# Kernel tuning notes

Measured on AMD Instinct MI355X. Metric: run time of the kernel, lower is better.

## Reference

```python
import jax, jax.numpy as jnp
import numpy as np

B, T, C, H = 2, 2048, 1024, 16
HD = C // H  # 64
EPS = 1e-5


def _ln(x, g, b):
    mu = jnp.mean(x, axis=-1, keepdims=True)
    var = jnp.var(x, axis=-1, keepdims=True)
    return (x - mu) * jax.lax.rsqrt(var + EPS) * g + b


def setup_inputs() -> dict:
    key = jax.random.key(0)
    ks = jax.random.split(key, 8)
    s = lambda n: 1.0 / np.sqrt(n)
    return {
        "x": jax.random.normal(ks[0], (B, T, C), dtype=jnp.float32),
        "ln1_g": jnp.ones((C,), jnp.float32), "ln1_b": jnp.zeros((C,), jnp.float32),
        "ln2_g": jnp.ones((C,), jnp.float32), "ln2_b": jnp.zeros((C,), jnp.float32),
        "w_in": jax.random.normal(ks[1], (C, 3 * C), jnp.float32) * s(C),
        "b_in": jnp.zeros((3 * C,), jnp.float32),
        "w_out": jax.random.normal(ks[2], (C, C), jnp.float32) * s(C),
        "b_out": jnp.zeros((C,), jnp.float32),
        "w_fc": jax.random.normal(ks[3], (C, 4 * C), jnp.float32) * s(C),
        "b_fc": jnp.zeros((4 * C,), jnp.float32),
        "w_proj": jax.random.normal(ks[4], (4 * C, C), jnp.float32) * s(4 * C),
        "b_proj": jnp.zeros((C,), jnp.float32),
    }


def reference(x, ln1_g, ln1_b, ln2_g, ln2_b, w_in, b_in, w_out, b_out,
              w_fc, b_fc, w_proj, b_proj):
    # --- residual 1: x + attn(ln1(x)) ---
    h = _ln(x, ln1_g, ln1_b)
    qkv = h @ w_in + b_in                          # (B,T,3C)
    # reshape to (B,T,H,3*HD) then chunk per head (matches torch code exactly)
    qkv = qkv.reshape(B, T, H, 3 * HD).transpose(0, 2, 1, 3)  # (B,H,T,3*HD)
    q, k, v = jnp.split(qkv, 3, axis=-1)           # each (B,H,T,HD)
    att = jnp.einsum('bhqd,bhkd->bhqk', q, k) / np.sqrt(HD)
    causal = jnp.tril(jnp.ones((T, T), bool))
    att = jnp.where(causal, att, -jnp.inf)
    att = jax.nn.softmax(att, axis=-1)
    o = jnp.einsum('bhqk,bhkd->bhqd', att, v)      # (B,H,T,HD)
    o = o.transpose(0, 2, 1, 3).reshape(B, T, C)
    x1 = x + (o @ w_out + b_out)
    # --- ln2 applied to residual stream, then residual 2 on top of ln2 output ---
    y = _ln(x1, ln2_g, ln2_b)
    mlp = jax.nn.gelu(y @ w_fc + b_fc, approximate=False) @ w_proj + b_proj
    return y + mlp
```

## Files before the change

kernel.cpp:

```cpp
#include <hip/hip_runtime.h>
#include <hip/hip_bf16.h>
#include <math.h>

typedef __bf16 bf16;
typedef __bf16 bf16x8 __attribute__((ext_vector_type(8)));
typedef __bf16 bf16x4 __attribute__((ext_vector_type(4)));
typedef float floatx4 __attribute__((ext_vector_type(4)));

#define B_ 2
#define T_ 2048
#define C_ 1024
#define H_ 16
#define HD_ 64


__device__ __forceinline__ void gload_lds16(const bf16* g, bf16* l) {
    __builtin_amdgcn_global_load_lds(
        (const __attribute__((address_space(1))) unsigned int*)(g),
        (__attribute__((address_space(3))) unsigned int*)(l), 16, 0, 0);
}

__global__ __launch_bounds__(256) void transpose_all(
        const float* __restrict__ w_in, const float* __restrict__ w_out,
        const float* __restrict__ w_fc, const float* __restrict__ w_proj,
        bf16* __restrict__ o_in, bf16* __restrict__ o_out,
        bf16* __restrict__ o_fc, bf16* __restrict__ o_proj) {
    __shared__ float shf[64 * 33];
    int t = blockIdx.x;
    int tid = threadIdx.x;
    if (t < 7168) {
        const float* src; bf16* dst; int K, N, idx;
        if (t < 3072) { src = w_in; dst = o_in; K = 1024; N = 3072; idx = t; }
        else          { src = w_fc; dst = o_fc; K = 1024; N = 4096; idx = t - 3072; }
        int ntx = N >> 5;
        int nt = (idx % ntx) * 32, kt = (idx / ntx) * 32;
        int tx = tid & 31, ty = tid >> 5;
        #pragma unroll
        for (int i = 0; i < 32; i += 8)
            shf[(ty + i) * 33 + tx] = src[(size_t)(kt + ty + i) * N + nt + tx];
        __syncthreads();
        #pragma unroll
        for (int i = 0; i < 32; i += 8)
            dst[(size_t)(nt + ty + i) * K + kt + tx] = (bf16)shf[tx * 33 + ty + i];
    } else {
        const float* src; bf16* dst; int K, idx;
        if (t < 7680) { src = w_out;  dst = o_out;  K = 1024; idx = t - 7168; }
        else          { src = w_proj; dst = o_proj; K = 4096; idx = t - 7680; }
        const int N = 1024;
        int n0 = (idx & 31) * 32, k0 = (idx >> 5) * 64;
        int col = tid & 31, kr = tid >> 5;
        #pragma unroll
        for (int s = 0; s < 8; s++)
            shf[(kr + s * 8) * 33 + col] = src[(size_t)(k0 + kr + s * 8) * N + n0 + col];
        __syncthreads();
        int tl = tid >> 6, l = tid & 63;
        int ntl = tl & 1, kcl = tl >> 1;
        int rr = ntl * 16 + (l & 15);
        int qd = l >> 4;
        bf16x8 v;
        #pragma unroll
        for (int e = 0; e < 8; e++)
            v[e] = (bf16)shf[(kcl * 32 + qd * 8 + e) * 33 + rr];
        size_t nt_g = (n0 >> 4) + ntl, kc_g = (k0 >> 5) + kcl;
        *(bf16x8*)(dst + (nt_g * (K >> 5) + kc_g) * 512 + l * 8) = v;
    }
}

__global__ __launch_bounds__(256) void ln_kernel(const float* __restrict__ x,
                                                 const float* __restrict__ g,
                                                 const float* __restrict__ b,
                                                 bf16* __restrict__ out_b,
                                                 float* __restrict__ out_f) {
    int row = blockIdx.x;
    int tid = threadIdx.x;
    const float* xr = x + (size_t)row * C_;
    float4 v = ((const float4*)xr)[tid];
    float s  = v.x + v.y + v.z + v.w;
    float ss = v.x * v.x + v.y * v.y + v.z * v.z + v.w * v.w;
    #pragma unroll
    for (int off = 32; off; off >>= 1) {
        s  += __shfl_down(s, off);
        ss += __shfl_down(ss, off);
    }
    __shared__ float red[8];
    int wid = tid >> 6;
    if ((tid & 63) == 0) { red[wid] = s; red[wid + 4] = ss; }
    __syncthreads();
    s  = red[0] + red[1] + red[2] + red[3];
    ss = red[4] + red[5] + red[6] + red[7];
    float mean = s * (1.0f / C_);
    float var  = ss * (1.0f / C_) - mean * mean;
    float rstd = rsqrtf(var + 1e-5f);
    float4 gv = ((const float4*)g)[tid];
    float4 bv = ((const float4*)b)[tid];
    float o0 = (v.x - mean) * rstd * gv.x + bv.x;
    float o1 = (v.y - mean) * rstd * gv.y + bv.y;
    float o2 = (v.z - mean) * rstd * gv.z + bv.z;
    float o3 = (v.w - mean) * rstd * gv.w + bv.w;
    bf16x4 ob = { (bf16)o0, (bf16)o1, (bf16)o2, (bf16)o3 };
    ((bf16x4*)out_b)[(size_t)row * 256 + tid] = ob;
    if (out_f) {
        float4 of; of.x = o0; of.y = o1; of.z = o2; of.w = o3;
        ((float4*)out_f)[(size_t)row * 256 + tid] = of;
    }
}

__device__ __forceinline__ float gelu_fast(float x) {
    float z2 = 1.5957691216f * (x + 0.044715f * x * x * x);
    float e = __expf(z2);
    float t = 1.0f - 2.0f * __builtin_amdgcn_rcpf(e + 1.0f);
    return 0.5f * x * (1.0f + t);
}

#define BAR() do { __builtin_amdgcn_sched_barrier(0); __builtin_amdgcn_s_barrier(); __builtin_amdgcn_sched_barrier(0); } while (0)
#define VMC6() asm volatile("s_waitcnt vmcnt(6)" ::: "memory")
#define VMC0() asm volatile("s_waitcnt vmcnt(0)" ::: "memory")

#define LOAD_A(AS, QM) \
  { _Pragma("unroll") for (int i_ = 0; i_ < 4; i_++) { \
      const int r_ = wm128 + ((QM) * 4 + i_) * 16 + lm; \
      _Pragma("unroll") for (int kc_ = 0; kc_ < 2; kc_++) \
        aR[i_][kc_] = *(const bf16x8*)((AS) + r_ * 64 + ((((kc_ << 2) | quad) ^ (lm & 7)) << 3)); } }

#define LOAD_B(BS, QN) \
  { _Pragma("unroll") for (int j_ = 0; j_ < 2; j_++) { \
      const int r_ = wn64 + ((QN) * 2 + j_) * 16 + lm; \
      _Pragma("unroll") for (int kc_ = 0; kc_ < 2; kc_++) \
        bR[QN][j_][kc_] = *(const bf16x8*)((BS) + r_ * 64 + ((((kc_ << 2) | quad) ^ (lm & 7)) << 3)); } }

#define MFMA_Q(QM, QN) \
  { __builtin_amdgcn_s_setprio(1); \
    _Pragma("unroll") for (int i_ = 0; i_ < 4; i_++) \
    _Pragma("unroll") for (int j_ = 0; j_ < 2; j_++) \
    _Pragma("unroll") for (int kc_ = 0; kc_ < 2; kc_++) \
      acc[(QM) * 4 + i_][(QN) * 2 + j_] = __builtin_amdgcn_mfma_f32_16x16x32_bf16( \
          aR[i_][kc_], bR[QN][j_][kc_], acc[(QM) * 4 + i_][(QN) * 2 + j_], 0, 0, 0); \
    __builtin_amdgcn_s_setprio(0); }

#define STG(gb, lb, r0v, k0v) \
    gload_lds16((gb) + (size_t)((r0v) + sr8) * K + (k0v) + scb, (lb) + ((r0v) + wid * 8) * 64)

template<int MODE>
__global__ __launch_bounds__(512, 2) void gemm256(const bf16* __restrict__ A,
                                                  const bf16* __restrict__ Bt,
                                                  const float* __restrict__ bias,
                                                  void* __restrict__ out,
                                                  int M, int N, int K) {
    (void)M;
    __shared__ __align__(16) bf16 smem[4 * 256 * 64];
    bf16* As0 = smem;
    bf16* Bs0 = smem + 1 * 256 * 64;
    bf16* As1 = smem + 2 * 256 * 64;
    bf16* Bs1 = smem + 3 * 256 * 64;

    int ntn = N >> 8;
    int lin = blockIdx.x;
    int id  = (lin & 7) * (gridDim.x >> 3) + (lin >> 3);
    int mt = id / ntn, nt = id - mt * ntn;
    int m0 = mt << 8, n0 = nt << 8;

    int tid = threadIdx.x;
    int wid = __builtin_amdgcn_readfirstlane(tid >> 6);
    int lane = tid & 63;
    int lm = lane & 15, quad = lane >> 4;
    int wm128 = (wid & 1) * 128;
    int wn64  = (wid >> 1) * 64;

    const bf16* Ablk = A  + (size_t)m0 * K;
    const bf16* Bblk = Bt + (size_t)n0 * K;

    int sr8 = wid * 8 + (lane >> 3);
    int scb = ((lane & 7) ^ (lane >> 3)) << 3;

    floatx4 acc[8][4];
    #pragma unroll
    for (int f = 0; f < 8; f++)
        #pragma unroll
        for (int g = 0; g < 4; g++) { floatx4 z = {0.f, 0.f, 0.f, 0.f}; acc[f][g] = z; }
    bf16x8 aR[4][2], bR[2][2][2];

    int nI = K >> 7;

    STG(Ablk, As0, 0, 0);   STG(Ablk, As0, 64, 0);
    STG(Ablk, As0, 128, 0); STG(Ablk, As0, 192, 0);
    STG(Bblk, Bs0, 0, 0);   STG(Bblk, Bs0, 64, 0);
    STG(Bblk, Bs0, 128, 0); STG(Bblk, Bs0, 192, 0);
    STG(Ablk, As1, 0, 64);  STG(Ablk, As1, 128, 64);
    STG(Bblk, Bs1, 0, 64);  STG(Bblk, Bs1, 64, 64);
    STG(Ablk, As1, 64, 64); STG(Ablk, As1, 192, 64);
    VMC6();
    BAR();

    for (int it = 0; it < nI; it++) {
        int kE = (2 * it + 2) << 6;
        int kO = (2 * it + 3) << 6;
        int kT = (2 * it + 1) << 6;
        bool nl = (it + 1 < nI);
        LOAD_A(As0, 0); LOAD_B(Bs0, 0);
        STG(Bblk, Bs1, 128, kT); STG(Bblk, Bs1, 192, kT);
        BAR(); MFMA_Q(0, 0); BAR();
        LOAD_B(Bs0, 1);
        if (nl) { STG(Ablk, As0, 0, kE); STG(Ablk, As0, 128, kE); }
        BAR(); MFMA_Q(0, 1); BAR();
        LOAD_A(As0, 1);
        if (nl) { STG(Bblk, Bs0, 0, kE); STG(Bblk, Bs0, 64, kE); }
        BAR(); MFMA_Q(1, 0); BAR();
        if (nl) { STG(Ablk, As0, 64, kE); STG(Ablk, As0, 192, kE); }
        BAR(); MFMA_Q(1, 1);
        if (nl) { VMC6(); } else { VMC0(); }
        BAR();
        LOAD_A(As1, 0); LOAD_B(Bs1, 0);
        if (nl) { STG(Bblk, Bs0, 128, kE); STG(Bblk, Bs0, 192, kE); }
        BAR(); MFMA_Q(0, 0); BAR();
        LOAD_B(Bs1, 1);
        if (nl) { STG(Ablk, As1, 0, kO); STG(Ablk, As1, 128, kO); }
        BAR(); MFMA_Q(0, 1); BAR();
        LOAD_A(As1, 1);
        if (nl) { STG(Bblk, Bs1, 0, kO); STG(Bblk, Bs1, 64, kO); }
        BAR(); MFMA_Q(1, 0); BAR();
        if (nl) { STG(Ablk, As1, 64, kO); STG(Ablk, As1, 192, kO); }
        BAR(); MFMA_Q(1, 1);
        if (nl) { VMC6(); }
        BAR();
    }

    if (MODE == 0) {
        bf16* ob = (bf16*)out;
        #pragma unroll
        for (int f = 0; f < 8; f++) {
            int row0 = m0 + wm128 + f * 16 + quad * 4;
            #pragma unroll
            for (int g = 0; g < 4; g++) {
                int n = n0 + wn64 + g * 16 + lm;
                float bsn = bias[n];
                #pragma unroll
                for (int r = 0; r < 4; r++)
                    ob[(size_t)(row0 + r) * N + n] = (bf16)(acc[f][g][r] + bsn);
            }
        }
    } else {
        bf16* ob = (bf16*)out;
        bf16* patch = smem + wid * (64 * 68);
        size_t mtb = (size_t)((m0 + wm128) >> 4);
        int ncb = (n0 + wn64) >> 5;
        #pragma unroll
        for (int h = 0; h < 2; h++) {
            #pragma unroll
            for (int ff = 0; ff < 4; ff++)
                #pragma unroll
                for (int g = 0; g < 4; g++) {
                    int n = n0 + wn64 + g * 16 + lm;
                    float bsn = bias[n];
                    #pragma unroll
                    for (int r = 0; r < 4; r++)
                        patch[(ff * 16 + quad * 4 + r) * 68 + g * 16 + lm] =
                            (bf16)gelu_fast(acc[h * 4 + ff][g][r] + bsn);
                }
            #pragma unroll
            for (int ff = 0; ff < 4; ff++)
                #pragma unroll
                for (int kc = 0; kc < 2; kc++) {
                    bf16x8 v = *(const bf16x8*)&patch[(ff * 16 + lm) * 68 + kc * 32 + quad * 8];
                    size_t tile = (mtb + h * 4 + ff) * (size_t)(N >> 5) + ncb + kc;
                    *(bf16x8*)(ob + tile * 512 + lane * 8) = v;
                }
        }
    }
}

#define GD_STEP(BUF, SS) \
  if ((SS) < S) { \
    int kp_ = 2 * (SS) + 4; \
    if (kp_ < KC) { \
      _Pragma("unroll") for (int i_ = 0; i_ < 4; i_++) \
        _Pragma("unroll") for (int c_ = 0; c_ < 2; c_++) \
          ab[((BUF) + 2) % 3][i_][c_] = *(const bf16x8*)(Ab + ((size_t)i_ * KC + kp_ + c_) * 512); \
      _Pragma("unroll") for (int j_ = 0; j_ < 2; j_++) \
        _Pragma("unroll") for (int c_ = 0; c_ < 2; c_++) \
          bb[((BUF) + 2) % 3][j_][c_] = *(const bf16x8*)(Bb + ((size_t)j_ * KC + kp_ + c_) * 512); \
    } \
    _Pragma("unroll") for (int c_ = 0; c_ < 2; c_++) \
      _Pragma("unroll") for (int i_ = 0; i_ < 4; i_++) \
        _Pragma("unroll") for (int j_ = 0; j_ < 2; j_++) \
          acc[i_][j_] = __builtin_amdgcn_mfma_f32_16x16x32_bf16(ab[BUF][i_][c_], bb[BUF][j_][c_], acc[i_][j_], 0, 0, 0); \
  }

__global__ __launch_bounds__(256, 2) void gemm_direct(const bf16* __restrict__ Af,
                                                      const bf16* __restrict__ Bf,
                                                      const float* __restrict__ bias,
                                                      const float* __restrict__ add,
                                                      float* __restrict__ out,
                                                      int M, int N, int K) {
    (void)M;
    int lin = blockIdx.x;
    int xcd = lin & 7, loc = lin >> 3;
    int m0 = ((xcd << 2) | (loc & 3)) * 128;
    int n0 = (loc >> 2) * 64;
    int tid = threadIdx.x;
    int wid = __builtin_amdgcn_readfirstlane(tid >> 6);
    int lane = tid & 63;
    int lm = lane & 15, quad = lane >> 4;
    int wm = (wid & 1) * 64, wn = (wid >> 1) * 32;
    int KC = K >> 5;
    const bf16* Ab = Af + ((size_t)((m0 + wm) >> 4) * KC) * 512 + lane * 8;
    const bf16* Bb = Bf + ((size_t)((n0 + wn) >> 4) * KC) * 512 + lane * 8;

    floatx4 acc[4][2];
    #pragma unroll
    for (int i = 0; i < 4; i++)
        #pragma unroll
        for (int j = 0; j < 2; j++) { floatx4 z = {0.f, 0.f, 0.f, 0.f}; acc[i][j] = z; }

    bf16x8 ab[3][4][2], bb[3][2][2];
    #pragma unroll
    for (int c = 0; c < 2; c++) {
        #pragma unroll
        for (int i = 0; i < 4; i++) {
            ab[0][i][c] = *(const bf16x8*)(Ab + ((size_t)i * KC + c) * 512);
            ab[1][i][c] = *(const bf16x8*)(Ab + ((size_t)i * KC + 2 + c) * 512);
        }
        #pragma unroll
        for (int j = 0; j < 2; j++) {
            bb[0][j][c] = *(const bf16x8*)(Bb + ((size_t)j * KC + c) * 512);
            bb[1][j][c] = *(const bf16x8*)(Bb + ((size_t)j * KC + 2 + c) * 512);
        }
    }

    int S = KC >> 1;
    for (int s0 = 0; s0 < S; s0 += 3) {
        GD_STEP(0, s0);
        GD_STEP(1, s0 + 1);
        GD_STEP(2, s0 + 2);
    }

    #pragma unroll
    for (int i = 0; i < 4; i++)
        #pragma unroll
        for (int j = 0; j < 2; j++) {
            int mbase = m0 + wm + i * 16 + quad * 4;
            int n     = n0 + wn + j * 16 + lm;
            float bsn = bias[n];
            #pragma unroll
            for (int r = 0; r < 4; r++) {
                size_t idx = (size_t)(mbase + r) * N + n;
                out[idx] = acc[i][j][r] + bsn + add[idx];
            }
        }
}

#define QT_ 128
#define KT_ 64

__global__ __launch_bounds__(512) void attn_mfma_kernel(const bf16* __restrict__ qkv,
                                                        bf16* __restrict__ of) {
    int bh = blockIdx.x;
    int b = bh >> 4, h = bh & 15;
    int q0 = (gridDim.y - 1 - blockIdx.y) * QT_;
    int tid = threadIdx.x, wid = tid >> 6, lane = tid & 63;
    int lm = lane & 15, quad = lane >> 4;
    int sw = lm & 7;
    int r0 = q0 + wid * 16;

    const bf16* base = qkv + (size_t)b * T_ * (3 * C_) + h * (3 * HD_);

    __shared__ __align__(16) bf16 Ks[KT_][72];
    __shared__ __align__(16) bf16 Vt[HD_][72];
    __shared__ __align__(16) bf16 PsT[8][16][64];

    bf16x8 qf[2];
    #pragma unroll
    for (int kc = 0; kc < 2; kc++) {
        bf16x8 t = *(const bf16x8*)(base + (size_t)(r0 + lm) * (3 * C_) + kc * 32 + quad * 8);
        #pragma unroll
        for (int e = 0; e < 8; e++) t[e] = (bf16)((float)t[e] * 0.125f);
        qf[kc] = t;
    }

    floatx4 acc_o[4];
    #pragma unroll
    for (int dn = 0; dn < 4; dn++) { floatx4 z = {0.f, 0.f, 0.f, 0.f}; acc_o[dn] = z; }
    float mst = -1e30f, lst = 0.0f;

    int srow = tid >> 3;
    int scol = (tid & 7) * 8;

    int kmax = q0 + QT_;
    for (int k0 = 0; k0 < kmax; k0 += KT_) {
        bf16x8 kv = *(const bf16x8*)(base + (size_t)(k0 + srow) * (3 * C_) + HD_ + scol);
        bf16x8 vv = *(const bf16x8*)(base + (size_t)(k0 + srow) * (3 * C_) + 2 * HD_ + scol);
        __syncthreads();
        *(bf16x8*)(&Ks[srow][scol]) = kv;
        {
            int c = scol >> 3;
            int pk = ((srow >> 3) ^ c) * 8 + (srow & 7);
            #pragma unroll
            for (int j = 0; j < 8; j++) Vt[scol + j][pk] = vv[j];
        }
        __syncthreads();

        if (k0 <= r0 + 15) {
            floatx4 st[4];
            #pragma unroll
            for (int bn = 0; bn < 4; bn++) { floatx4 z = {0.f, 0.f, 0.f, 0.f}; st[bn] = z; }
            #pragma unroll
            for (int kc = 0; kc < 2; kc++) {
                bf16x8 kf[4];
                #pragma unroll
                for (int bn = 0; bn < 4; bn++)
                    kf[bn] = *(const bf16x8*)(&Ks[bn * 16 + lm][kc * 32 + quad * 8]);
                #pragma unroll
                for (int bn = 0; bn < 4; bn++)
                    st[bn] = __builtin_amdgcn_mfma_f32_16x16x32_bf16(kf[bn], qf[kc], st[bn], 0, 0, 0);
            }

            float vv_[4][4];
            float rm = -1e30f;
            if (k0 + KT_ - 1 > r0) {
                int gq = r0 + lm;
                #pragma unroll
                for (int bn = 0; bn < 4; bn++)
                    #pragma unroll
                    for (int r = 0; r < 4; r++) {
                        int key = k0 + bn * 16 + quad * 4 + r;
                        float sv = (key <= gq) ? st[bn][r] : -1e30f;
                        vv_[bn][r] = sv;
                        rm = fmaxf(rm, sv);
                    }
            } else {
                #pragma unroll
                for (int bn = 0; bn < 4; bn++)
                    #pragma unroll
                    for (int r = 0; r < 4; r++) {
                        vv_[bn][r] = st[bn][r];
                        rm = fmaxf(rm, st[bn][r]);
                    }
            }
            rm = fmaxf(rm, __shfl_xor(rm, 16));
            rm = fmaxf(rm, __shfl_xor(rm, 32));
            float mnew = fmaxf(mst, rm);
            float alpha = __expf(mst - mnew);
            mst = mnew;
            float ps = 0.f;
            #pragma unroll
            for (int bn = 0; bn < 4; bn++) {
                float p0 = __expf(vv_[bn][0] - mnew);
                float p1 = __expf(vv_[bn][1] - mnew);
                float p2 = __expf(vv_[bn][2] - mnew);
                float p3 = __expf(vv_[bn][3] - mnew);
                ps += (p0 + p1) + (p2 + p3);
                bf16x4 pk = { (bf16)p0, (bf16)p1, (bf16)p2, (bf16)p3 };
                int kb = bn * 2 + (quad >> 1);
                int col = ((kb ^ sw) << 3) + (quad & 1) * 4;
                *(bf16x4*)(&PsT[wid][lm][col]) = pk;
            }
            ps += __shfl_xor(ps, 16);
            ps += __shfl_xor(ps, 32);
            lst = lst * alpha + ps;

            #pragma unroll
            for (int r = 0; r < 4; r++) {
                float ar = __shfl(alpha, quad * 4 + r);
                #pragma unroll
                for (int dn = 0; dn < 4; dn++) acc_o[dn][r] *= ar;
            }

            __asm__ volatile("s_waitcnt lgkmcnt(0)" ::: "memory");

            #pragma unroll
            for (int kc = 0; kc < 2; kc++) {
                bf16x8 pa = *(const bf16x8*)(&PsT[wid][lm][((kc * 4 + quad) ^ sw) << 3]);
                bf16x8 vfr[4];
                #pragma unroll
                for (int dn = 0; dn < 4; dn++) {
                    int d = dn * 16 + lm;
                    int swd = (d >> 3) & 7;
                    vfr[dn] = *(const bf16x8*)(&Vt[d][(((kc * 4 + quad) ^ swd) << 3)]);
                }
                #pragma unroll
                for (int dn = 0; dn < 4; dn++)
                    acc_o[dn] = __builtin_amdgcn_mfma_f32_16x16x32_bf16(pa, vfr[dn], acc_o[dn], 0, 0, 0);
            }
        }
    }

    float il = 1.0f / lst;
    #pragma unroll
    for (int r = 0; r < 4; r++) {
        float ir = __shfl(il, quad * 4 + r);
        #pragma unroll
        for (int dn = 0; dn < 4; dn++)
            PsT[wid][quad * 4 + r][dn * 16 + lm] = (bf16)(acc_o[dn][r] * ir);
    }
    __asm__ volatile("s_waitcnt lgkmcnt(0)" ::: "memory");
    size_t mtb = ((size_t)b * T_ + r0) >> 4;
    #pragma unroll
    for (int kcl = 0; kcl < 2; kcl++) {
        bf16x8 v = *(const bf16x8*)&PsT[wid][lm][kcl * 32 + quad * 8];
        *(bf16x8*)(of + (mtb * (C_ >> 5) + (h * 2 + kcl)) * 512 + lane * 8) = v;
    }
}

extern "C" void kernel_launch(void* const* d_in, const int* in_sizes, int n_in,
                              void* d_out, int out_size, void* d_ws, size_t ws_size,
                              hipStream_t stream) {
    (void)in_sizes; (void)n_in; (void)out_size; (void)ws_size;
    const float* x      = (const float*)d_in[0];
    const float* ln1_g  = (const float*)d_in[1];
    const float* ln1_b  = (const float*)d_in[2];
    const float* ln2_g  = (const float*)d_in[3];
    const float* ln2_b  = (const float*)d_in[4];
    const float* w_in   = (const float*)d_in[5];
    const float* b_in   = (const float*)d_in[6];
    const float* w_out  = (const float*)d_in[7];
    const float* b_out  = (const float*)d_in[8];
    const float* w_fc   = (const float*)d_in[9];
    const float* b_fc   = (const float*)d_in[10];
    const float* w_proj = (const float*)d_in[11];
    const float* b_proj = (const float*)d_in[12];

    char* ws = (char*)d_ws;
    const size_t MB = 1024 * 1024;
    bf16*  w_inT   = (bf16*)(ws + 0);
    bf16*  w_outF  = (bf16*)(ws + 6 * MB);
    bf16*  w_fcT   = (bf16*)(ws + 8 * MB);
    bf16*  w_projF = (bf16*)(ws + 16 * MB);
    bf16*  qkv     = (bf16*)(ws + 24 * MB);
    bf16*  fc_frag = (bf16*)(ws + 24 * MB);
    bf16*  o_frag  = (bf16*)(ws + 56 * MB);
    bf16*  y_b     = (bf16*)(ws + 56 * MB);
    bf16*  h_b     = (bf16*)(ws + 64 * MB);
    float* x1      = (float*)(ws + 64 * MB);
    float* y_f     = (float*)(ws + 80 * MB);

    const int M = B_ * T_;

    transpose_all<<<9728, 256, 0, stream>>>(w_in, w_out, w_fc, w_proj,
                                            w_inT, w_outF, w_fcT, w_projF);

    ln_kernel<<<M, 256, 0, stream>>>(x, ln1_g, ln1_b, h_b, nullptr);
    gemm256<0><<<(M >> 8) * ((3 * C_) >> 8), 512, 0, stream>>>(h_b, w_inT, b_in,
                                                               qkv, M, 3 * C_, C_);
    attn_mfma_kernel<<<dim3(B_ * H_, T_ / QT_), 512, 0, stream>>>(qkv, o_frag);
    gemm_direct<<<512, 256, 0, stream>>>(o_frag, w_outF, b_out, x, x1, M, C_, C_);
    ln_kernel<<<M, 256, 0, stream>>>(x1, ln2_g, ln2_b, y_b, y_f);
    gemm256<1><<<(M >> 8) * ((4 * C_) >> 8), 512, 0, stream>>>(y_b, w_fcT, b_fc,
                                                               fc_frag, M, 4 * C_, C_);
    gemm_direct<<<512, 256, 0, stream>>>(fc_frag, w_projF, b_proj, y_f,
                                         (float*)d_out, M, C_, 4 * C_);
}
```

Baseline: 330.0 us.

## Replace fragment-layout direct GEMM with LDS-pipelined row-major GEMM for out/proj

Drops the pre-swizzled MFMA fragment layout for the attention output, FC activations and the w_out/w_proj weights, and stores them all row-major. The two N=1024 GEMMs now use a new kernel that streams A and B through a 4-stage LDS ring filled by global_load_lds, uses XOR-swizzled reads and 128x128 tiles with 512 threads. It also raises wave priority around the MFMA blocks in both the GEMM and the attention kernel. The intent is to hide global-load latency behind compute and cut the register-resident pipeline pressure of the old direct kernel, at the cost of LDS traffic and a barrier every K step.

```diff
diff --git a/kernel.cpp b/kernel.cpp
--- a/kernel.cpp
+++ b/kernel.cpp
@@ -13,7 +13,6 @@
 #define H_ 16
 #define HD_ 64
 
-
 __device__ __forceinline__ void gload_lds16(const bf16* g, bf16* l) {
     __builtin_amdgcn_global_load_lds(
         (const __attribute__((address_space(1))) unsigned int*)(g),
@@ -25,45 +24,24 @@
         const float* __restrict__ w_fc, const float* __restrict__ w_proj,
         bf16* __restrict__ o_in, bf16* __restrict__ o_out,
         bf16* __restrict__ o_fc, bf16* __restrict__ o_proj) {
-    __shared__ float shf[64 * 33];
+    __shared__ float shf[32 * 33];
     int t = blockIdx.x;
     int tid = threadIdx.x;
-    if (t < 7168) {
-        const float* src; bf16* dst; int K, N, idx;
-        if (t < 3072) { src = w_in; dst = o_in; K = 1024; N = 3072; idx = t; }
-        else          { src = w_fc; dst = o_fc; K = 1024; N = 4096; idx = t - 3072; }
-        int ntx = N >> 5;
-        int nt = (idx % ntx) * 32, kt = (idx / ntx) * 32;
-        int tx = tid & 31, ty = tid >> 5;
-        #pragma unroll
-        for (int i = 0; i < 32; i += 8)
-            shf[(ty + i) * 33 + tx] = src[(size_t)(kt + ty + i) * N + nt + tx];
-        __syncthreads();
-        #pragma unroll
-        for (int i = 0; i < 32; i += 8)
-            dst[(size_t)(nt + ty + i) * K + kt + tx] = (bf16)shf[tx * 33 + ty + i];
-    } else {
-        const float* src; bf16* dst; int K, idx;
-        if (t < 7680) { src = w_out;  dst = o_out;  K = 1024; idx = t - 7168; }
-        else          { src = w_proj; dst = o_proj; K = 4096; idx = t - 7680; }
-        const int N = 1024;
-        int n0 = (idx & 31) * 32, k0 = (idx >> 5) * 64;
-        int col = tid & 31, kr = tid >> 5;
-        #pragma unroll
-        for (int s = 0; s < 8; s++)
-            shf[(kr + s * 8) * 33 + col] = src[(size_t)(k0 + kr + s * 8) * N + n0 + col];
-        __syncthreads();
-        int tl = tid >> 6, l = tid & 63;
-        int ntl = tl & 1, kcl = tl >> 1;
-        int rr = ntl * 16 + (l & 15);
-        int qd = l >> 4;
-        bf16x8 v;
-        #pragma unroll
-        for (int e = 0; e < 8; e++)
-            v[e] = (bf16)shf[(kcl * 32 + qd * 8 + e) * 33 + rr];
-        size_t nt_g = (n0 >> 4) + ntl, kc_g = (k0 >> 5) + kcl;
-        *(bf16x8*)(dst + (nt_g * (K >> 5) + kc_g) * 512 + l * 8) = v;
-    }
+    const float* src; bf16* dst; int K, N, idx;
+    if (t < 3072)      { src = w_in;   dst = o_in;   K = 1024; N = 3072; idx = t; }
+    else if (t < 7168) { src = w_fc;   dst = o_fc;   K = 1024; N = 4096; idx = t - 3072; }
+    else if (t < 8192) { src = w_out;  dst = o_out;  K = 1024; N = 1024; idx = t - 7168; }
+    else               { src = w_proj; dst = o_proj; K = 4096; N = 1024; idx = t - 8192; }
+    int ntx = N >> 5;
+    int nt = (idx % ntx) * 32, kt = (idx / ntx) * 32;
+    int tx = tid & 31, ty = tid >> 5;
+    #pragma unroll
+    for (int i = 0; i < 32; i += 8)
+        shf[(ty + i) * 33 + tx] = src[(size_t)(kt + ty + i) * N + nt + tx];
+    __syncthreads();
+    #pragma unroll
+    for (int i = 0; i < 32; i += 8)
+        dst[(size_t)(nt + ty + i) * K + kt + tx] = (bf16)shf[tx * 33 + ty + i];
 }
 
 __global__ __launch_bounds__(256) void ln_kernel(const float* __restrict__ x,
@@ -241,8 +219,6 @@
     } else {
         bf16* ob = (bf16*)out;
         bf16* patch = smem + wid * (64 * 68);
-        size_t mtb = (size_t)((m0 + wm128) >> 4);
-        int ncb = (n0 + wn64) >> 5;
         #pragma unroll
         for (int h = 0; h < 2; h++) {
             #pragma unroll
@@ -261,84 +237,91 @@
                 #pragma unroll
                 for (int kc = 0; kc < 2; kc++) {
                     bf16x8 v = *(const bf16x8*)&patch[(ff * 16 + lm) * 68 + kc * 32 + quad * 8];
-                    size_t tile = (mtb + h * 4 + ff) * (size_t)(N >> 5) + ncb + kc;
-                    *(bf16x8*)(ob + tile * 512 + lane * 8) = v;
+                    size_t row = (size_t)(m0 + wm128 + h * 64 + ff * 16 + lm);
+                    *(bf16x8*)(ob + row * N + n0 + wn64 + kc * 32 + quad * 8) = v;
                 }
         }
     }
 }
 
-#define GD_STEP(BUF, SS) \
-  if ((SS) < S) { \
-    int kp_ = 2 * (SS) + 4; \
-    if (kp_ < KC) { \
-      _Pragma("unroll") for (int i_ = 0; i_ < 4; i_++) \
-        _Pragma("unroll") for (int c_ = 0; c_ < 2; c_++) \
-          ab[((BUF) + 2) % 3][i_][c_] = *(const bf16x8*)(Ab + ((size_t)i_ * KC + kp_ + c_) * 512); \
-      _Pragma("unroll") for (int j_ = 0; j_ < 2; j_++) \
-        _Pragma("unroll") for (int c_ = 0; c_ < 2; c_++) \
-          bb[((BUF) + 2) % 3][j_][c_] = *(const bf16x8*)(Bb + ((size_t)j_ * KC + kp_ + c_) * 512); \
-    } \
-    _Pragma("unroll") for (int c_ = 0; c_ < 2; c_++) \
-      _Pragma("unroll") for (int i_ = 0; i_ < 4; i_++) \
-        _Pragma("unroll") for (int j_ = 0; j_ < 2; j_++) \
-          acc[i_][j_] = __builtin_amdgcn_mfma_f32_16x16x32_bf16(ab[BUF][i_][c_], bb[BUF][j_][c_], acc[i_][j_], 0, 0, 0); \
-  }
-
-__global__ __launch_bounds__(256, 2) void gemm_direct(const bf16* __restrict__ Af,
-                                                      const bf16* __restrict__ Bf,
-                                                      const float* __restrict__ bias,
-                                                      const float* __restrict__ add,
-                                                      float* __restrict__ out,
-                                                      int M, int N, int K) {
-    (void)M;
+#define VMCP(n) asm volatile("s_waitcnt vmcnt(" #n ")" ::: "memory")
+
+#define STGP(kt) { bf16* bs_ = smem + ((kt) & 3) * 16384; \
+    gload_lds16(Ab + (size_t)sr8 * K + (kt) * 64 + scb,        bs_ + (wid * 8) * 64); \
+    gload_lds16(Ab + (size_t)(64 + sr8) * K + (kt) * 64 + scb, bs_ + (64 + wid * 8) * 64); \
+    gload_lds16(Bb + (size_t)sr8 * K + (kt) * 64 + scb,        bs_ + 8192 + (wid * 8) * 64); \
+    gload_lds16(Bb + (size_t)(64 + sr8) * K + (kt) * 64 + scb, bs_ + 8192 + (64 + wid * 8) * 64); }
+
+__global__ __launch_bounds__(512, 2) void gemm_npipe(const bf16* __restrict__ A,
+                                                     const bf16* __restrict__ Bt,
+                                                     const float* __restrict__ bias,
+                                                     const float* __restrict__ add,
+                                                     float* __restrict__ out,
+                                                     int N, int K) {
+    __shared__ __align__(16) bf16 smem[4 * 16384];
     int lin = blockIdx.x;
     int xcd = lin & 7, loc = lin >> 3;
-    int m0 = ((xcd << 2) | (loc & 3)) * 128;
-    int n0 = (loc >> 2) * 64;
+    int m0 = (xcd * 4 + (loc & 3)) * 128;
+    int n0 = (loc >> 2) * 128;
     int tid = threadIdx.x;
     int wid = __builtin_amdgcn_readfirstlane(tid >> 6);
     int lane = tid & 63;
     int lm = lane & 15, quad = lane >> 4;
-    int wm = (wid & 1) * 64, wn = (wid >> 1) * 32;
-    int KC = K >> 5;
-    const bf16* Ab = Af + ((size_t)((m0 + wm) >> 4) * KC) * 512 + lane * 8;
-    const bf16* Bb = Bf + ((size_t)((n0 + wn) >> 4) * KC) * 512 + lane * 8;
-
-    floatx4 acc[4][2];
-    #pragma unroll
-    for (int i = 0; i < 4; i++)
-        #pragma unroll
-        for (int j = 0; j < 2; j++) { floatx4 z = {0.f, 0.f, 0.f, 0.f}; acc[i][j] = z; }
-
-    bf16x8 ab[3][4][2], bb[3][2][2];
-    #pragma unroll
-    for (int c = 0; c < 2; c++) {
-        #pragma unroll
-        for (int i = 0; i < 4; i++) {
-            ab[0][i][c] = *(const bf16x8*)(Ab + ((size_t)i * KC + c) * 512);
-            ab[1][i][c] = *(const bf16x8*)(Ab + ((size_t)i * KC + 2 + c) * 512);
-        }
-        #pragma unroll
-        for (int j = 0; j < 2; j++) {
-            bb[0][j][c] = *(const bf16x8*)(Bb + ((size_t)j * KC + c) * 512);
-            bb[1][j][c] = *(const bf16x8*)(Bb + ((size_t)j * KC + 2 + c) * 512);
-        }
-    }
-
-    int S = KC >> 1;
-    for (int s0 = 0; s0 < S; s0 += 3) {
-        GD_STEP(0, s0);
-        GD_STEP(1, s0 + 1);
-        GD_STEP(2, s0 + 2);
-    }
-
-    #pragma unroll
-    for (int i = 0; i < 4; i++)
-        #pragma unroll
-        for (int j = 0; j < 2; j++) {
-            int mbase = m0 + wm + i * 16 + quad * 4;
-            int n     = n0 + wn + j * 16 + lm;
+    int wm32 = (wid & 3) * 32, wn64 = (wid >> 2) * 64;
+    int sr8 = wid * 8 + (lane >> 3);
+    int scb = ((lane & 7) ^ (lane >> 3)) << 3;
+    const bf16* Ab = A  + (size_t)m0 * K;
+    const bf16* Bb = Bt + (size_t)n0 * K;
+    int NT = K >> 6;
+
+    floatx4 acc[2][4];
+    #pragma unroll
+    for (int i = 0; i < 2; i++)
+        #pragma unroll
+        for (int j = 0; j < 4; j++) { floatx4 z = {0.f, 0.f, 0.f, 0.f}; acc[i][j] = z; }
+    bf16x8 aR[2][2], bR[4][2];
+
+    STGP(0); STGP(1); STGP(2);
+    VMCP(8);
+    BAR();
+
+    for (int t = 0; t < NT; t++) {
+        if (t + 3 < NT) STGP(t + 3);
+        bf16* bs = smem + (t & 3) * 16384;
+        #pragma unroll
+        for (int i = 0; i < 2; i++)
+            #pragma unroll
+            for (int kc = 0; kc < 2; kc++)
+                aR[i][kc] = *(const bf16x8*)(bs + (wm32 + i * 16 + lm) * 64 +
+                                             ((((kc << 2) | quad) ^ (lm & 7)) << 3));
+        #pragma unroll
+        for (int j = 0; j < 4; j++)
+            #pragma unroll
+            for (int kc = 0; kc < 2; kc++)
+                bR[j][kc] = *(const bf16x8*)(bs + 8192 + (wn64 + j * 16 + lm) * 64 +
+                                             ((((kc << 2) | quad) ^ (lm & 7)) << 3));
+        __builtin_amdgcn_s_setprio(1);
+        #pragma unroll
+        for (int kc = 0; kc < 2; kc++)
+            #pragma unroll
+            for (int i = 0; i < 2; i++)
+                #pragma unroll
+                for (int j = 0; j < 4; j++)
+                    acc[i][j] = __builtin_amdgcn_mfma_f32_16x16x32_bf16(
+                        aR[i][kc], bR[j][kc], acc[i][j], 0, 0, 0);
+        __builtin_amdgcn_s_setprio(0);
+        if (t + 3 < NT)      { VMCP(8); }
+        else if (t == NT - 3){ VMCP(4); }
+        else if (t == NT - 2){ VMCP(0); }
+        BAR();
+    }
+
+    #pragma unroll
+    for (int i = 0; i < 2; i++)
+        #pragma unroll
+        for (int j = 0; j < 4; j++) {
+            int mbase = m0 + wm32 + i * 16 + quad * 4;
+            int n     = n0 + wn64 + j * 16 + lm;
             float bsn = bias[n];
             #pragma unroll
             for (int r = 0; r < 4; r++) {
@@ -408,9 +391,11 @@
                 #pragma unroll
                 for (int bn = 0; bn < 4; bn++)
                     kf[bn] = *(const bf16x8*)(&Ks[bn * 16 + lm][kc * 32 + quad * 8]);
+                __builtin_amdgcn_s_setprio(1);
                 #pragma unroll
                 for (int bn = 0; bn < 4; bn++)
                     st[bn] = __builtin_amdgcn_mfma_f32_16x16x32_bf16(kf[bn], qf[kc], st[bn], 0, 0, 0);
+                __builtin_amdgcn_s_setprio(0);
             }
 
             float vv_[4][4];
@@ -476,9 +461,11 @@
                     int swd = (d >> 3) & 7;
                     vfr[dn] = *(const bf16x8*)(&Vt[d][(((kc * 4 + quad) ^ swd) << 3)]);
                 }
+                __builtin_amdgcn_s_setprio(1);
                 #pragma unroll
                 for (int dn = 0; dn < 4; dn++)
                     acc_o[dn] = __builtin_amdgcn_mfma_f32_16x16x32_bf16(pa, vfr[dn], acc_o[dn], 0, 0, 0);
+                __builtin_amdgcn_s_setprio(0);
             }
         }
     }
@@ -492,11 +479,11 @@
             PsT[wid][quad * 4 + r][dn * 16 + lm] = (bf16)(acc_o[dn][r] * ir);
     }
     __asm__ volatile("s_waitcnt lgkmcnt(0)" ::: "memory");
-    size_t mtb = ((size_t)b * T_ + r0) >> 4;
+    size_t rowg = (size_t)b * T_ + r0 + lm;
     #pragma unroll
     for (int kcl = 0; kcl < 2; kcl++) {
         bf16x8 v = *(const bf16x8*)&PsT[wid][lm][kcl * 32 + quad * 8];
-        *(bf16x8*)(of + (mtb * (C_ >> 5) + (h * 2 + kcl)) * 512 + lane * 8) = v;
+        *(bf16x8*)(of + rowg * C_ + h * HD_ + kcl * 32 + quad * 8) = v;
     }
 }
 
@@ -521,12 +508,12 @@
     char* ws = (char*)d_ws;
     const size_t MB = 1024 * 1024;
     bf16*  w_inT   = (bf16*)(ws + 0);
-    bf16*  w_outF  = (bf16*)(ws + 6 * MB);
+    bf16*  w_outT  = (bf16*)(ws + 6 * MB);
     bf16*  w_fcT   = (bf16*)(ws + 8 * MB);
-    bf16*  w_projF = (bf16*)(ws + 16 * MB);
+    bf16*  w_projT = (bf16*)(ws + 16 * MB);
     bf16*  qkv     = (bf16*)(ws + 24 * MB);
-    bf16*  fc_frag = (bf16*)(ws + 24 * MB);
-    bf16*  o_frag  = (bf16*)(ws + 56 * MB);
+    bf16*  fc_b    = (bf16*)(ws + 24 * MB);
+    bf16*  o_b     = (bf16*)(ws + 56 * MB);
     bf16*  y_b     = (bf16*)(ws + 56 * MB);
     bf16*  h_b     = (bf16*)(ws + 64 * MB);
     float* x1      = (float*)(ws + 64 * MB);
@@ -534,17 +521,17 @@
 
     const int M = B_ * T_;
 
-    transpose_all<<<9728, 256, 0, stream>>>(w_in, w_out, w_fc, w_proj,
-                                            w_inT, w_outF, w_fcT, w_projF);
+    transpose_all<<<12288, 256, 0, stream>>>(w_in, w_out, w_fc, w_proj,
+                                             w_inT, w_outT, w_fcT, w_projT);
 
     ln_kernel<<<M, 256, 0, stream>>>(x, ln1_g, ln1_b, h_b, nullptr);
     gemm256<0><<<(M >> 8) * ((3 * C_) >> 8), 512, 0, stream>>>(h_b, w_inT, b_in,
                                                                qkv, M, 3 * C_, C_);
-    attn_mfma_kernel<<<dim3(B_ * H_, T_ / QT_), 512, 0, stream>>>(qkv, o_frag);
-    gemm_direct<<<512, 256, 0, stream>>>(o_frag, w_outF, b_out, x, x1, M, C_, C_);
+    attn_mfma_kernel<<<dim3(B_ * H_, T_ / QT_), 512, 0, stream>>>(qkv, o_b);
+    gemm_npipe<<<256, 512, 0, stream>>>(o_b, w_outT, b_out, x, x1, C_, C_);
     ln_kernel<<<M, 256, 0, stream>>>(x1, ln2_g, ln2_b, y_b, y_f);
     gemm256<1><<<(M >> 8) * ((4 * C_) >> 8), 512, 0, stream>>>(y_b, w_fcT, b_fc,
-                                                               fc_frag, M, 4 * C_, C_);
-    gemm_direct<<<512, 256, 0, stream>>>(fc_frag, w_projF, b_proj, y_f,
-                                         (float*)d_out, M, C_, 4 * C_);
-}
+                                                               fc_b, M, 4 * C_, C_);
+    gemm_npipe<<<256, 512, 0, stream>>>(fc_b, w_projT, b_proj, y_f,
+                                        (float*)d_out, C_, 4 * C_);
+}
```

Measured after the change: 319.6 us. 1.03x faster.
